# Optimization experiments

Measured on AMD Instinct MI355X. Metric: run time of the kernel, lower is better.

## Reference

```python
import jax, jax.numpy as jnp
import numpy as np

N, E, IN, H, OUT = 100000, 1600000, 64, 64, 10
NEG_SLOPE = 0.2  # PyG GATConv default negative_slope


def _glorot(key, shape):
    fan = sum(shape) if len(shape) > 1 else shape[0]
    return jax.random.normal(key, shape, dtype=jnp.float32) * jnp.sqrt(2.0 / fan)


def setup_inputs() -> dict:
    key = jax.random.key(0)
    ks = jax.random.split(key, 16)
    x = jax.random.normal(ks[0], (N, IN), dtype=jnp.float32)
    edge_index = jax.random.randint(ks[1], (2, E), 0, N, dtype=jnp.int32)
    dims = [(IN, H), (H, H), (H, OUT)]
    params = {}
    for i, (fi, fo) in enumerate(dims, start=1):
        params[f"W{i}"] = _glorot(ks[4 * i - 2], (fi, fo))
        params[f"a{i}s"] = _glorot(ks[4 * i - 1], (fo,))
        params[f"a{i}d"] = _glorot(ks[4 * i], (fo,))
        params[f"b{i}"] = jnp.zeros((fo,), dtype=jnp.float32)
    return {"x": x, "edge_index": edge_index, **params}


def gat_conv(x, src, dst, W, a_s, a_d, b):
    """Single-head GATConv (PyG defaults): gather -> leaky_relu scores ->
    segment softmax over dst -> scatter-add aggregate."""
    n = x.shape[0]
    h = x @ W                                   # [N, Fo]
    alpha_src = h @ a_s                          # [N]
    alpha_dst = h @ a_d                          # [N]
    e = jax.nn.leaky_relu(alpha_src[src] + alpha_dst[dst], NEG_SLOPE)  # [E']
    m = jax.ops.segment_max(e, dst, num_segments=n)                    # stable softmax max
    ex = jnp.exp(e - m[dst])
    denom = jax.ops.segment_sum(ex, dst, num_segments=n)
    alpha = ex / denom[dst]                      # [E'] per-dst softmax
    out = jax.ops.segment_sum(alpha[:, None] * h[src], dst, num_segments=n)
    return out + b


def reference(x, edge_index, W1, a1s, a1d, b1, W2, a2s, a2d, b2, W3, a3s, a3d, b3):
    n = x.shape[0]
    loops = jnp.arange(n, dtype=edge_index.dtype)  # add_self_loops=True
    src = jnp.concatenate([edge_index[0], loops])
    dst = jnp.concatenate([edge_index[1], loops])
    h = jax.nn.relu(gat_conv(x, src, dst, W1, a1s, a1d, b1))
    # dropout is identity at inference (training=False)
    h = jax.nn.relu(gat_conv(h, src, dst, W2, a2s, a2d, b2))
    h = gat_conv(h, src, dst, W3, a3s, a3d, b3)
    return jax.nn.log_softmax(h, axis=1)
```

## Files before the change

kernel.cpp:

```cpp
#include <hip/hip_runtime.h>
#include <math.h>
#include <type_traits>


#define NEG_SLOPE 0.2f
#define BKT_BITS 9
#define BKT_SZ   512
#define PACK_SRC_BITS 20

typedef _Float16 h8v __attribute__((ext_vector_type(8)));
typedef _Float16 h4v __attribute__((ext_vector_type(4)));
typedef float f4v __attribute__((ext_vector_type(4)));

__global__ __launch_bounds__(512) void k_bscan(const int* __restrict__ bcount, int nb,
                                               int E, int N, int* __restrict__ ebase,
                                               int* __restrict__ gcur,
                                               int* __restrict__ rowptr) {
    __shared__ int sm[BKT_SZ];
    int t = threadIdx.x;
    int v = (t < nb) ? bcount[t] : 0;
    sm[t] = v;
    __syncthreads();
    for (int o = 1; o < BKT_SZ; o <<= 1) {
        int tv = (t >= o) ? sm[t - o] : 0;
        __syncthreads();
        sm[t] += tv;
        __syncthreads();
    }
    int excl = sm[t] - v;
    if (t < nb) {
        ebase[t] = excl;
        gcur[t] = excl;
    }
    if (t == nb - 1) ebase[nb] = excl + v;
    if (t == 0) rowptr[N] = E + N;
}

__global__ __launch_bounds__(1024) void k_bscatter(const int* __restrict__ src,
                                                   const int* __restrict__ dst, int E,
                                                   int nb, int* __restrict__ gcur,
                                                   int* __restrict__ ebuf) {
    __shared__ int lc[BKT_SZ];
    __shared__ int gb[BKT_SZ];
    for (int i = threadIdx.x; i < nb; i += 1024) lc[i] = 0;
    __syncthreads();
    int base = blockIdx.x * 8192;
    int bkt[8], rnk[8], pk[8];
#pragma unroll
    for (int j = 0; j < 8; j++) {
        int i = base + j * 1024 + threadIdx.x;
        bkt[j] = -1;
        if (i < E) {
            int d = dst[i];
            int s = src[i];
            int b = d >> BKT_BITS;
            bkt[j] = b;
            rnk[j] = atomicAdd(&lc[b], 1);
            pk[j] = ((d & (BKT_SZ - 1)) << PACK_SRC_BITS) | s;
        }
    }
    __syncthreads();
    for (int b = threadIdx.x; b < nb; b += 1024)
        if (lc[b]) gb[b] = atomicAdd(&gcur[b], lc[b]);
    __syncthreads();
#pragma unroll
    for (int j = 0; j < 8; j++)
        if (bkt[j] >= 0) ebuf[gb[bkt[j]] + rnk[j]] = pk[j];
}

__global__ __launch_bounds__(512) void k_bcsr(const int* __restrict__ ebuf,
                                              const int* __restrict__ ebase, int N,
                                              int* __restrict__ rowptr,
                                              int* __restrict__ csr) {
    __shared__ int cnt[BKT_SZ];
    __shared__ int sm[BKT_SZ];
    int b = blockIdx.x;
    int t = threadIdx.x;
    int n0 = b << BKT_BITS;
    int nn = min(BKT_SZ, N - n0);
    cnt[t] = 0;
    __syncthreads();
    int e0 = ebase[b], e1 = ebase[b + 1];
    for (int i = e0 + t; i < e1; i += BKT_SZ)
        atomicAdd(&cnt[ebuf[i] >> PACK_SRC_BITS], 1);
    __syncthreads();
    int v = cnt[t] + (t < nn ? 1 : 0);
    sm[t] = v;
    __syncthreads();
    for (int o = 1; o < BKT_SZ; o <<= 1) {
        int tv = (t >= o) ? sm[t - o] : 0;
        __syncthreads();
        sm[t] += tv;
        __syncthreads();
    }
    int excl = sm[t] - v;
    int cb = e0 + n0;
    if (t < nn) {
        rowptr[n0 + t] = cb + excl;
        csr[cb + excl] = n0 + t;
    }
    cnt[t] = excl + 1;
    __syncthreads();
    for (int i = e0 + t; i < e1; i += BKT_SZ) {
        int p = ebuf[i];
        int dl = p >> PACK_SRC_BITS;
        int pos = atomicAdd(&cnt[dl], 1);
        csr[cb + pos] = p & ((1 << PACK_SRC_BITS) - 1);
    }
}

__device__ __forceinline__ void gemm64_body(
    int bid, int nblocks, const float* __restrict__ X, const float* __restrict__ W,
    const float* __restrict__ a_s, const float* __restrict__ a_d, int N,
    _Float16* __restrict__ H, float* __restrict__ asb, float* __restrict__ adb) {
    constexpr int NT = 4;
    int lane = threadIdx.x & 63;
    int quad = lane >> 4;
    int c16 = lane & 15;

    h8v bf[NT][2];
    float asv[NT], adv[NT];
#pragma unroll
    for (int nt = 0; nt < NT; nt++) {
        int n = nt * 16 + c16;
        asv[nt] = a_s[n];
        adv[nt] = a_d[n];
#pragma unroll
        for (int kt = 0; kt < 2; kt++)
#pragma unroll
            for (int j = 0; j < 8; j++) {
                int k = kt * 32 + quad * 8 + j;
                bf[nt][kt][j] = (_Float16)W[k * 64 + n];
            }
    }

    int wid = (bid * 256 + (int)threadIdx.x) >> 6;
    int nw = (nblocks * 256) >> 6;
    int ntile = (N + 15) >> 4;

    for (int t = wid; t < ntile; t += nw) {
        int m0 = t << 4;
        int row = m0 + c16;
        const float* xr = X + (size_t)min(row, N - 1) * 64;
        h8v af[2];
#pragma unroll
        for (int kt = 0; kt < 2; kt++) {
            f4v x0 = *(const f4v*)(xr + kt * 32 + quad * 8);
            f4v x1 = *(const f4v*)(xr + kt * 32 + quad * 8 + 4);
#pragma unroll
            for (int j = 0; j < 4; j++) {
                af[kt][j] = (_Float16)x0[j];
                af[kt][4 + j] = (_Float16)x1[j];
            }
        }
        f4v c[NT];
#pragma unroll
        for (int nt = 0; nt < NT; nt++) c[nt] = (f4v){0.f, 0.f, 0.f, 0.f};
#pragma unroll
        for (int kt = 0; kt < 2; kt++)
#pragma unroll
            for (int nt = 0; nt < NT; nt++)
                c[nt] = __builtin_amdgcn_mfma_f32_16x16x32_f16(af[kt], bf[nt][kt],
                                                               c[nt], 0, 0, 0);
#pragma unroll
        for (int reg = 0; reg < 4; reg++) {
            int r = m0 + quad * 4 + reg;
            if (r < N) {
#pragma unroll
                for (int nt = 0; nt < NT; nt++)
                    H[(size_t)r * 64 + nt * 16 + c16] = (_Float16)c[nt][reg];
            }
        }
        float ps[4], pd[4];
#pragma unroll
        for (int reg = 0; reg < 4; reg++) {
            ps[reg] = 0.f;
            pd[reg] = 0.f;
#pragma unroll
            for (int nt = 0; nt < NT; nt++) {
                ps[reg] = fmaf(c[nt][reg], asv[nt], ps[reg]);
                pd[reg] = fmaf(c[nt][reg], adv[nt], pd[reg]);
            }
        }
        for (int o = 1; o < 16; o <<= 1) {
#pragma unroll
            for (int reg = 0; reg < 4; reg++) {
                ps[reg] += __shfl_xor(ps[reg], o, 64);
                pd[reg] += __shfl_xor(pd[reg], o, 64);
            }
        }
        if (c16 == 0) {
#pragma unroll
            for (int reg = 0; reg < 4; reg++) {
                int r = m0 + quad * 4 + reg;
                if (r < N) {
                    asb[r] = ps[reg];
                    adb[r] = pd[reg];
                }
            }
        }
    }
}

__global__ __launch_bounds__(256) void k_hist_gemm(
    const int* __restrict__ dst, int E, int nb, int* __restrict__ bcount,
    int histBlocks,
    const float* __restrict__ X, const float* __restrict__ W,
    const float* __restrict__ a_s, const float* __restrict__ a_d, int N,
    _Float16* __restrict__ H, float* __restrict__ asb, float* __restrict__ adb) {
    __shared__ int h[BKT_SZ];
    int bid = blockIdx.x;
    if (bid < histBlocks) {
        for (int i = threadIdx.x; i < nb; i += 256) h[i] = 0;
        __syncthreads();
        for (int i = bid * 256 + threadIdx.x; i < E; i += histBlocks * 256)
            atomicAdd(&h[dst[i] >> BKT_BITS], 1);
        __syncthreads();
        for (int i = threadIdx.x; i < nb; i += 256)
            if (h[i]) atomicAdd(&bcount[i], h[i]);
    } else {
        gemm64_body(bid - histBlocks, (int)gridDim.x - histBlocks, X, W, a_s, a_d,
                    N, H, asb, adb);
    }
}

template <int FP, typename InT>
__global__ __launch_bounds__(256) void k_gemm(
    const InT* __restrict__ X, const float* __restrict__ W,
    const float* __restrict__ a_s, const float* __restrict__ a_d,
    int N, int Freal,
    _Float16* __restrict__ H, float* __restrict__ asb, float* __restrict__ adb) {
    constexpr int NT = FP / 16;
    int lane = threadIdx.x & 63;
    int quad = lane >> 4;
    int c16 = lane & 15;

    h8v bf[NT][2];
    float asv[NT], adv[NT];
#pragma unroll
    for (int nt = 0; nt < NT; nt++) {
        int n = nt * 16 + c16;
        bool ok = (n < Freal);
        asv[nt] = ok ? a_s[n] : 0.f;
        adv[nt] = ok ? a_d[n] : 0.f;
#pragma unroll
        for (int kt = 0; kt < 2; kt++)
#pragma unroll
            for (int j = 0; j < 8; j++) {
                int k = kt * 32 + quad * 8 + j;
                bf[nt][kt][j] = (_Float16)(ok ? W[k * Freal + n] : 0.f);
            }
    }

    int wid = (blockIdx.x * blockDim.x + threadIdx.x) >> 6;
    int nw = (gridDim.x * blockDim.x) >> 6;
    int ntile = (N + 15) >> 4;

    for (int t = wid; t < ntile; t += nw) {
        int m0 = t << 4;
        int row = m0 + c16;
        const InT* xr = X + (size_t)min(row, N - 1) * 64;
        h8v af[2];
        if constexpr (std::is_same<InT, float>::value) {
#pragma unroll
            for (int kt = 0; kt < 2; kt++) {
                f4v x0 = *(const f4v*)(xr + kt * 32 + quad * 8);
                f4v x1 = *(const f4v*)(xr + kt * 32 + quad * 8 + 4);
#pragma unroll
                for (int j = 0; j < 4; j++) {
                    af[kt][j] = (_Float16)x0[j];
                    af[kt][4 + j] = (_Float16)x1[j];
                }
            }
        } else {
#pragma unroll
            for (int kt = 0; kt < 2; kt++)
                af[kt] = *(const h8v*)(xr + kt * 32 + quad * 8);
        }
        f4v c[NT];
#pragma unroll
        for (int nt = 0; nt < NT; nt++) c[nt] = (f4v){0.f, 0.f, 0.f, 0.f};
#pragma unroll
        for (int kt = 0; kt < 2; kt++)
#pragma unroll
            for (int nt = 0; nt < NT; nt++)
                c[nt] = __builtin_amdgcn_mfma_f32_16x16x32_f16(af[kt], bf[nt][kt],
                                                               c[nt], 0, 0, 0);
#pragma unroll
        for (int reg = 0; reg < 4; reg++) {
            int r = m0 + quad * 4 + reg;
            if (r < N) {
#pragma unroll
                for (int nt = 0; nt < NT; nt++)
                    H[(size_t)r * FP + nt * 16 + c16] = (_Float16)c[nt][reg];
            }
        }
        float ps[4], pd[4];
#pragma unroll
        for (int reg = 0; reg < 4; reg++) {
            ps[reg] = 0.f;
            pd[reg] = 0.f;
#pragma unroll
            for (int nt = 0; nt < NT; nt++) {
                ps[reg] = fmaf(c[nt][reg], asv[nt], ps[reg]);
                pd[reg] = fmaf(c[nt][reg], adv[nt], pd[reg]);
            }
        }
        for (int o = 1; o < 16; o <<= 1) {
#pragma unroll
            for (int reg = 0; reg < 4; reg++) {
                ps[reg] += __shfl_xor(ps[reg], o, 64);
                pd[reg] += __shfl_xor(pd[reg], o, 64);
            }
        }
        if (c16 == 0) {
#pragma unroll
            for (int reg = 0; reg < 4; reg++) {
                int r = m0 + quad * 4 + reg;
                if (r < N) {
                    asb[r] = ps[reg];
                    adb[r] = pd[reg];
                }
            }
        }
    }
}

template <int FP>
__device__ __forceinline__ void agg_slow(
    int node, const _Float16* __restrict__ H, const float* __restrict__ asb,
    const float* __restrict__ adb, const float* __restrict__ bias,
    const int* __restrict__ rowptr, const int* __restrict__ csr,
    int N, int Freal, void* __restrict__ out, int mode, int lane) {
    if (node >= N) return;
    int start = rowptr[node];
    int end = rowptr[node + 1];
    float ad = adb[node];
    int lf = lane & (FP - 1);
    const float NEG_INF = -__builtin_inff();

    float m = NEG_INF;
    for (int base = start; base < end; base += 64) {
        int i = base + lane;
        if (i < end) {
            float t = asb[csr[i]] + ad;
            float e = (t > 0.f) ? t : NEG_SLOPE * t;
            m = fmaxf(m, e);
        }
    }
    for (int o = 32; o > 0; o >>= 1) m = fmaxf(m, __shfl_xor(m, o, 64));
    float dsum = 0.f, acc = 0.f;
    for (int base = start; base < end; base += 64) {
        int i = base + lane;
        int cnt = min(64, end - base);
        int s = 0;
        float p = 0.f;
        if (i < end) {
            s = csr[i];
            float t = asb[s] + ad;
            float e = (t > 0.f) ? t : NEG_SLOPE * t;
            p = __expf(e - m);
        }
        dsum += p;
        for (int j = 0; j < cnt; j++) {
            float pj = __shfl(p, j, 64);
            int sj = __shfl(s, j, 64);
            acc = fmaf(pj, (float)H[(size_t)sj * FP + lf], acc);
        }
    }
    for (int o = 32; o > 0; o >>= 1) dsum += __shfl_xor(dsum, o, 64);

    float b = (lf < Freal) ? bias[lf] : 0.f;
    float z = acc / dsum + b;
    if (mode == 0) {
        if (lane < FP)
            ((_Float16*)out)[(size_t)node * FP + lane] = (_Float16)fmaxf(z, 0.f);
    } else {
        float zz = (lane < Freal) ? z : NEG_INF;
        float zm = zz;
        for (int o = 32; o > 0; o >>= 1) zm = fmaxf(zm, __shfl_xor(zm, o, 64));
        float ez = (lane < Freal) ? __expf(zz - zm) : 0.f;
        float es = ez;
        for (int o = 32; o > 0; o >>= 1) es += __shfl_xor(es, o, 64);
        if (lane < Freal)
            ((float*)out)[(size_t)node * Freal + lane] = zz - zm - __logf(es);
    }
}

template <int FP, int W>
__global__ __launch_bounds__(256) void k_agg(
    const _Float16* __restrict__ H, const float* __restrict__ asb,
    const float* __restrict__ adb, const float* __restrict__ bias,
    const int* __restrict__ rowptr, const int* __restrict__ csr,
    int N, int Freal, void* __restrict__ out, int mode) {
    constexpr int LPR = FP / W;
    constexpr int GRPH = 32 / LPR;
    constexpr int MAXIT = 32 / GRPH;
    using vecW = typename std::conditional<W == 8, h8v, h4v>::type;
    int lane = threadIdx.x & 63;
    int half = lane >> 5;
    int li = lane & 31;
    int wid = (blockIdx.x * blockDim.x + threadIdx.x) >> 6;
    int nA = 2 * wid;
    if (nA >= N) return;
    int n = nA + half;
    bool valid = (n < N);
    int start = 0, end = 0;
    float ad = 0.f;
    if (valid) {
        start = rowptr[n];
        end = rowptr[n + 1];
        ad = adb[n];
    }
    int deg = end - start;
    int degm = max(deg, __shfl_xor(deg, 32, 64));

    const float NEG_INF = -__builtin_inff();

    if (degm <= 32) {
        int g = li / LPR;
        int fl = li % LPR;
        bool have = (li < deg);
        int s = 0;
        if (have) s = csr[start + li];
        float as_v = have ? asb[s] : 0.f;

        vecW r[MAXIT];
        int gidx = half * 32 + g;
#pragma unroll
        for (int it = 0; it < MAXIT; ++it) {
            if (it * GRPH < degm) {
                int sj = __shfl(s, gidx + it * GRPH, 64);
                r[it] = ((const vecW*)(H + (size_t)sj * FP))[fl];
            }
        }

        float e = NEG_INF;
        if (have) {
            float t = as_v + ad;
            e = (t > 0.f) ? t : NEG_SLOPE * t;
        }
        float m = e;
        for (int o = 16; o > 0; o >>= 1) m = fmaxf(m, __shfl_xor(m, o, 64));
        float p = have ? __expf(e - m) : 0.f;

        float acc[W];
#pragma unroll
        for (int c = 0; c < W; c++) acc[c] = 0.f;
#pragma unroll
        for (int it = 0; it < MAXIT; ++it) {
            if (it * GRPH < degm) {
                float pj = __shfl(p, gidx + it * GRPH, 64);
#pragma unroll
                for (int c = 0; c < W; c++)
                    acc[c] = fmaf(pj, (float)r[it][c], acc[c]);
            }
        }

        float dsum = p;
        for (int o = 16; o > 0; o >>= 1) dsum += __shfl_xor(dsum, o, 64);

        for (int o = LPR; o < 32; o <<= 1) {
#pragma unroll
            for (int c = 0; c < W; c++) acc[c] += __shfl_xor(acc[c], o, 64);
        }
        float inv = 1.f / dsum;
        int fbase = fl * W;

        if (mode == 0) {
            if (valid && li < LPR) {
                vecW zh;
#pragma unroll
                for (int c = 0; c < W; c++)
                    zh[c] = (_Float16)fmaxf(fmaf(acc[c], inv, bias[fbase + c]), 0.f);
                ((vecW*)((_Float16*)out + (size_t)n * FP))[fl] = zh;
            }
        } else {
            float zc[W];
#pragma unroll
            for (int c = 0; c < W; c++) {
                int f = fbase + c;
                zc[c] = (f < Freal) ? fmaf(acc[c], inv, bias[f]) : NEG_INF;
            }
            float vm = zc[0];
#pragma unroll
            for (int c = 1; c < W; c++) vm = fmaxf(vm, zc[c]);
            for (int o = 1; o < LPR; o <<= 1) vm = fmaxf(vm, __shfl_xor(vm, o, 64));
            float es = 0.f;
#pragma unroll
            for (int c = 0; c < W; c++) es += __expf(zc[c] - vm);
            for (int o = 1; o < LPR; o <<= 1) es += __shfl_xor(es, o, 64);
            float ls = __logf(es);
            if (valid && li < LPR) {
#pragma unroll
                for (int c = 0; c < W; c++) {
                    int f = fbase + c;
                    if (f < Freal)
                        ((float*)out)[(size_t)n * Freal + f] = zc[c] - vm - ls;
                }
            }
        }
    } else {
        agg_slow<FP>(nA, H, asb, adb, bias, rowptr, csr, N, Freal, out, mode, lane);
        agg_slow<FP>(nA + 1, H, asb, adb, bias, rowptr, csr, N, Freal, out, mode, lane);
    }
}

extern "C" void kernel_launch(void* const* d_in, const int* in_sizes, int n_in,
                              void* d_out, int out_size, void* d_ws, size_t ws_size,
                              hipStream_t stream) {
    const float* x = (const float*)d_in[0];
    const int* ei = (const int*)d_in[1];
    const float* W1 = (const float*)d_in[2];
    const float* a1s = (const float*)d_in[3];
    const float* a1d = (const float*)d_in[4];
    const float* b1 = (const float*)d_in[5];
    const float* W2 = (const float*)d_in[6];
    const float* a2s = (const float*)d_in[7];
    const float* a2d = (const float*)d_in[8];
    const float* b2 = (const float*)d_in[9];
    const float* W3 = (const float*)d_in[10];
    const float* a3s = (const float*)d_in[11];
    const float* a3d = (const float*)d_in[12];
    const float* b3 = (const float*)d_in[13];

    const int N = in_sizes[0] / 64;
    const int E = in_sizes[1] / 2;
    const int Etot = E + N;
    const int nb = (N + BKT_SZ - 1) >> BKT_BITS;
    const int* srcv = ei;
    const int* dstv = ei + E;

    size_t off = 0;
    char* base = (char*)d_ws;
    auto carve = [&](size_t bytes) -> void* {
        void* p = base + off;
        off = (off + bytes + 255) & ~(size_t)255;
        return p;
    };
    int* bcount = (int*)carve((size_t)(nb + 1) * 4);
    int* ebase = (int*)carve((size_t)(nb + 1) * 4);
    int* gcur = (int*)carve((size_t)nb * 4);
    int* rowptr = (int*)carve((size_t)(N + 1) * 4);
    int* csr = (int*)carve((size_t)Etot * 4);
    float* asb = (float*)carve((size_t)N * 4);
    float* adb = (float*)carve((size_t)N * 4);
    _Float16* hA = (_Float16*)carve((size_t)N * 64 * 2);
    _Float16* fB = (_Float16*)carve((size_t)N * 64 * 2);
    _Float16* hC = (_Float16*)carve((size_t)N * 16 * 2);
    int* ebuf = (int*)carve((size_t)E * 4);

    const int aggBlocks = (N + 7) / 8;
    const int gemmBlocks = 784;
    const int histBlocks = 512;

    hipMemsetAsync(bcount, 0, (size_t)nb * 4, stream);
    k_hist_gemm<<<histBlocks + gemmBlocks, 256, 0, stream>>>(
        dstv, E, nb, bcount, histBlocks, x, W1, a1s, a1d, N, hA, asb, adb);
    k_bscan<<<1, BKT_SZ, 0, stream>>>(bcount, nb, E, N, ebase, gcur, rowptr);
    k_bscatter<<<(E + 8191) / 8192, 1024, 0, stream>>>(srcv, dstv, E, nb, gcur, ebuf);
    k_bcsr<<<nb, BKT_SZ, 0, stream>>>(ebuf, ebase, N, rowptr, csr);

    k_agg<64, 8><<<aggBlocks, 256, 0, stream>>>(hA, asb, adb, b1, rowptr, csr, N, 64,
                                                (void*)fB, 0);
    k_gemm<64, _Float16><<<gemmBlocks, 256, 0, stream>>>(fB, W2, a2s, a2d, N, 64, hA,
                                                         asb, adb);
    k_agg<64, 8><<<aggBlocks, 256, 0, stream>>>(hA, asb, adb, b2, rowptr, csr, N, 64,
                                                (void*)fB, 0);
    k_gemm<16, _Float16><<<gemmBlocks, 256, 0, stream>>>(fB, W3, a3s, a3d, N, 10, hC,
                                                         asb, adb);
    k_agg<16, 4><<<aggBlocks, 256, 0, stream>>>(hC, asb, adb, b3, rowptr, csr, N, 10,
                                                d_out, 1);
}
```

Before: 320.5 us.

## Fuse layer-3 linear projection and attention scores into layer-2 aggregation epilogue

The second aggregation kernel now computes the layer-3 feature transform (64->10) and the source/destination attention logits in its epilogue, using W3 staged in shared memory and cross-lane shuffle reductions. The separate k_gemm launch for layer 3 and the round trip of the 64-wide fp16 layer-2 output through global memory go away. Separate asb/adb buffers are added so the fused kernel does not overwrite logits that other nodes are still reading. In exchange the epilogue carries extra shuffles, registers and per-block shared-memory setup.

```diff
diff --git a/kernel.cpp b/kernel.cpp
--- a/kernel.cpp
+++ b/kernel.cpp
@@ -326,12 +326,15 @@
     }
 }
 
-template <int FP>
+template <int FP, bool FUSE>
 __device__ __forceinline__ void agg_slow(
     int node, const _Float16* __restrict__ H, const float* __restrict__ asb,
     const float* __restrict__ adb, const float* __restrict__ bias,
     const int* __restrict__ rowptr, const int* __restrict__ csr,
-    int N, int Freal, void* __restrict__ out, int mode, int lane) {
+    int N, int Freal, void* __restrict__ out, int mode, int lane,
+    const float* w3l, const float* s3a, const float* s3d,
+    _Float16* __restrict__ hCout, float* __restrict__ asbN,
+    float* __restrict__ adbN) {
     if (node >= N) return;
     int start = rowptr[node];
     int end = rowptr[node + 1];
@@ -373,8 +376,39 @@
     float b = (lf < Freal) ? bias[lf] : 0.f;
     float z = acc / dsum + b;
     if (mode == 0) {
-        if (lane < FP)
-            ((_Float16*)out)[(size_t)node * FP + lane] = (_Float16)fmaxf(z, 0.f);
+        float zr = fmaxf(z, 0.f);
+        if constexpr (FUSE) {
+            float p3[10];
+#pragma unroll
+            for (int k = 0; k < 10; k++) p3[k] = zr * w3l[lf * 11 + k];
+            for (int o = 1; o < 64; o <<= 1) {
+#pragma unroll
+                for (int k = 0; k < 10; k++) p3[k] += __shfl_xor(p3[k], o, 64);
+            }
+            float as3 = 0.f, ad3 = 0.f;
+#pragma unroll
+            for (int k = 0; k < 10; k++) {
+                as3 = fmaf(p3[k], s3a[k], as3);
+                ad3 = fmaf(p3[k], s3d[k], ad3);
+            }
+            if (lane == 0) {
+                asbN[node] = as3;
+                adbN[node] = ad3;
+                h8v lo, hi;
+#pragma unroll
+                for (int k = 0; k < 8; k++) lo[k] = (_Float16)p3[k];
+                hi[0] = (_Float16)p3[8];
+                hi[1] = (_Float16)p3[9];
+#pragma unroll
+                for (int k = 2; k < 8; k++) hi[k] = (_Float16)0.f;
+                h8v* hp = (h8v*)(hCout + (size_t)node * 16);
+                hp[0] = lo;
+                hp[1] = hi;
+            }
+        } else {
+            if (lane < FP)
+                ((_Float16*)out)[(size_t)node * FP + lane] = (_Float16)zr;
+        }
     } else {
         float zz = (lane < Freal) ? z : NEG_INF;
         float zm = zz;
@@ -387,16 +421,35 @@
     }
 }
 
-template <int FP, int W>
+template <int FP, int W, bool FUSE>
 __global__ __launch_bounds__(256) void k_agg(
     const _Float16* __restrict__ H, const float* __restrict__ asb,
     const float* __restrict__ adb, const float* __restrict__ bias,
     const int* __restrict__ rowptr, const int* __restrict__ csr,
-    int N, int Freal, void* __restrict__ out, int mode) {
+    int N, int Freal, void* __restrict__ out, int mode,
+    const float* __restrict__ W3g, const float* __restrict__ a3sg,
+    const float* __restrict__ a3dg, _Float16* __restrict__ hCout,
+    float* __restrict__ asbN, float* __restrict__ adbN) {
     constexpr int LPR = FP / W;
     constexpr int GRPH = 32 / LPR;
     constexpr int MAXIT = 32 / GRPH;
     using vecW = typename std::conditional<W == 8, h8v, h4v>::type;
+
+    __shared__ float w3l[FUSE ? 64 * 11 : 1];
+    __shared__ float s3a[FUSE ? 16 : 1];
+    __shared__ float s3d[FUSE ? 16 : 1];
+    if constexpr (FUSE) {
+        for (int i = threadIdx.x; i < 640; i += 256) {
+            int c = i / 10, k = i - c * 10;
+            w3l[c * 11 + k] = W3g[i];
+        }
+        if (threadIdx.x < 10) {
+            s3a[threadIdx.x] = a3sg[threadIdx.x];
+            s3d[threadIdx.x] = a3dg[threadIdx.x];
+        }
+        __syncthreads();
+    }
+
     int lane = threadIdx.x & 63;
     int half = lane >> 5;
     int li = lane & 31;
@@ -468,12 +521,54 @@
         int fbase = fl * W;
 
         if (mode == 0) {
-            if (valid && li < LPR) {
-                vecW zh;
+            if constexpr (FUSE) {
+                float z[W];
 #pragma unroll
                 for (int c = 0; c < W; c++)
-                    zh[c] = (_Float16)fmaxf(fmaf(acc[c], inv, bias[fbase + c]), 0.f);
-                ((vecW*)((_Float16*)out + (size_t)n * FP))[fl] = zh;
+                    z[c] = fmaxf(fmaf(acc[c], inv, bias[fbase + c]), 0.f);
+                float p3[10];
+#pragma unroll
+                for (int k = 0; k < 10; k++) {
+                    float t = 0.f;
+#pragma unroll
+                    for (int j = 0; j < W; j++)
+                        t = fmaf(z[j], w3l[(fbase + j) * 11 + k], t);
+                    p3[k] = t;
+                }
+                for (int o = 1; o < LPR; o <<= 1) {
+#pragma unroll
+                    for (int k = 0; k < 10; k++)
+                        p3[k] += __shfl_xor(p3[k], o, 64);
+                }
+                float as3 = 0.f, ad3 = 0.f;
+#pragma unroll
+                for (int k = 0; k < 10; k++) {
+                    as3 = fmaf(p3[k], s3a[k], as3);
+                    ad3 = fmaf(p3[k], s3d[k], ad3);
+                }
+                if (valid && li == 0) {
+                    asbN[n] = as3;
+                    adbN[n] = ad3;
+                    h8v lo, hi;
+#pragma unroll
+                    for (int k = 0; k < 8; k++) lo[k] = (_Float16)p3[k];
+                    hi[0] = (_Float16)p3[8];
+                    hi[1] = (_Float16)p3[9];
+#pragma unroll
+                    for (int k = 2; k < 8; k++) hi[k] = (_Float16)0.f;
+                    h8v* hp = (h8v*)(hCout + (size_t)n * 16);
+                    hp[0] = lo;
+                    hp[1] = hi;
+                }
+            } else {
+                if (valid && li < LPR) {
+                    vecW zh;
+#pragma unroll
+                    for (int c = 0; c < W; c++)
+                        zh[c] = (_Float16)fmaxf(fmaf(acc[c], inv, bias[fbase + c]),
+                                                0.f);
+                    ((vecW*)((_Float16*)out + (size_t)n * FP))[fl] = zh;
+                }
             }
         } else {
             float zc[W];
@@ -501,8 +596,10 @@
             }
         }
     } else {
-        agg_slow<FP>(nA, H, asb, adb, bias, rowptr, csr, N, Freal, out, mode, lane);
-        agg_slow<FP>(nA + 1, H, asb, adb, bias, rowptr, csr, N, Freal, out, mode, lane);
+        agg_slow<FP, FUSE>(nA, H, asb, adb, bias, rowptr, csr, N, Freal, out,
+                           mode, lane, w3l, s3a, s3d, hCout, asbN, adbN);
+        agg_slow<FP, FUSE>(nA + 1, H, asb, adb, bias, rowptr, csr, N, Freal, out,
+                           mode, lane, w3l, s3a, s3d, hCout, asbN, adbN);
     }
 }
 
@@ -545,6 +642,8 @@
     int* csr = (int*)carve((size_t)Etot * 4);
     float* asb = (float*)carve((size_t)N * 4);
     float* adb = (float*)carve((size_t)N * 4);
+    float* asbB = (float*)carve((size_t)N * 4);
+    float* adbB = (float*)carve((size_t)N * 4);
     _Float16* hA = (_Float16*)carve((size_t)N * 64 * 2);
     _Float16* fB = (_Float16*)carve((size_t)N * 64 * 2);
     _Float16* hC = (_Float16*)carve((size_t)N * 16 * 2);
@@ -561,14 +660,15 @@
     k_bscatter<<<(E + 8191) / 8192, 1024, 0, stream>>>(srcv, dstv, E, nb, gcur, ebuf);
     k_bcsr<<<nb, BKT_SZ, 0, stream>>>(ebuf, ebase, N, rowptr, csr);
 
-    k_agg<64, 8><<<aggBlocks, 256, 0, stream>>>(hA, asb, adb, b1, rowptr, csr, N, 64,
-                                                (void*)fB, 0);
+    k_agg<64, 8, false><<<aggBlocks, 256, 0, stream>>>(
+        hA, asb, adb, b1, rowptr, csr, N, 64, (void*)fB, 0,
+        nullptr, nullptr, nullptr, nullptr, nullptr, nullptr);
     k_gemm<64, _Float16><<<gemmBlocks, 256, 0, stream>>>(fB, W2, a2s, a2d, N, 64, hA,
                                                          asb, adb);
-    k_agg<64, 8><<<aggBlocks, 256, 0, stream>>>(hA, asb, adb, b2, rowptr, csr, N, 64,
-                                                (void*)fB, 0);
-    k_gemm<16, _Float16><<<gemmBlocks, 256, 0, stream>>>(fB, W3, a3s, a3d, N, 10, hC,
-                                                         asb, adb);
-    k_agg<16, 4><<<aggBlocks, 256, 0, stream>>>(hC, asb, adb, b3, rowptr, csr, N, 10,
-                                                d_out, 1);
-}
+    k_agg<64, 8, true><<<aggBlocks, 256, 0, stream>>>(
+        hA, asb, adb, b2, rowptr, csr, N, 64, nullptr, 0,
+        W3, a3s, a3d, hC, asbB, adbB);
+    k_agg<16, 4, false><<<aggBlocks, 256, 0, stream>>>(
+        hC, asbB, adbB, b3, rowptr, csr, N, 10, d_out, 1,
+        nullptr, nullptr, nullptr, nullptr, nullptr, nullptr);
+}
```

Measured after the change: 342.3 us. 6.8% more time.
